# Kernel tuning notes

Measured on AMD Instinct MI355X. Metric: run time of the kernel, lower is better.

## Reference

```python
import jax, jax.numpy as jnp
import numpy as np

B, C, L = 32, 8, 2048
K, S = 512, 64  # num_shapelets, shapelets_size


def setup_inputs() -> dict:
    key = jax.random.key(0)
    k1, k2 = jax.random.split(key)
    x = jax.random.normal(k1, (B, C, L), dtype=jnp.float32)
    shapelets = jax.random.normal(k2, (C, K, S), dtype=jnp.float32)
    return {"x": x, "shapelets": shapelets}


def reference(x, shapelets):
    # x: [B, C, L]; shapelets: [C, K, S]
    s = shapelets.shape[-1]
    n_dims = x.shape[1]
    W = x.shape[2] - s + 1  # number of sliding windows
    # unfold(2, S, 1): gather overlapping windows -> [B, C, W, S]
    idx = jnp.arange(W)[:, None] + jnp.arange(s)[None, :]
    xw = x[:, :, idx]
    # L2-normalize windows along window length (clamp min like torch)
    xw = xw / jnp.maximum(jnp.linalg.norm(xw, axis=-1, keepdims=True), 1e-8)
    # L2-normalize shapelets along length
    sn = shapelets / jnp.maximum(jnp.linalg.norm(shapelets, axis=-1, keepdims=True), 1e-8)
    # matmul [B,C,W,S] @ [C,S,K] then sum over C, fused into one einsum -> [B, W, K]
    sim = jnp.einsum('bcws,cks->bwk', xw, sn) / n_dims
    sim = jax.nn.relu(sim)
    # max over window positions -> [B, K]; keep the singleton channel dim like torch ([B,1,K])
    out = jnp.max(sim, axis=1)
    return out[:, None, :]
```

## Files before the change

### kernel.cpp

```cpp
#include <hip/hip_runtime.h>


#define B_ 32
#define C_ 8
#define L_ 2048
#define K_ 512
#define S_ 64
#define W_ 1985
#define TW 64

typedef _Float16 f16x8 __attribute__((ext_vector_type(8)));
typedef float f32x4 __attribute__((ext_vector_type(4)));
typedef float f32x4u __attribute__((ext_vector_type(4), aligned(4)));

__global__ __launch_bounds__(256)
void prep_k(const float* __restrict__ x, const float* __restrict__ sh,
            _Float16* __restrict__ Bp, float* __restrict__ invn,
            float* __restrict__ out) {
    __shared__ float xr[L_];
    const int tid = threadIdx.x;
    const int blk = blockIdx.x;

    if (blk < 128) {
        const int sb   = blk * 4 + (tid >> 6);
        const int c    = sb >> 6;
        const int ks   = (sb >> 5) & 1;
        const int nt   = sb & 31;
        const int lane = tid & 63;
        const int ncol = lane & 15, quad = lane >> 4;
        const int q    = nt * 16 + ncol;

        const float4* sp = (const float4*)(sh + (size_t)(c * K_ + q) * S_);
        float ss = 0.f;
        #pragma unroll
        for (int i = 0; i < 4; ++i) {
            float4 v = sp[quad * 4 + i];
            ss += v.x * v.x + v.y * v.y + v.z * v.z + v.w * v.w;
        }
        ss += __shfl_xor(ss, 16);
        ss += __shfl_xor(ss, 32);
        float inv = 1.f / fmaxf(sqrtf(ss), 1e-8f);

        float4 u0 = sp[ks * 8 + quad * 2];
        float4 u1 = sp[ks * 8 + quad * 2 + 1];
        f16x8 o;
        o[0] = (_Float16)(u0.x * inv); o[1] = (_Float16)(u0.y * inv);
        o[2] = (_Float16)(u0.z * inv); o[3] = (_Float16)(u0.w * inv);
        o[4] = (_Float16)(u1.x * inv); o[5] = (_Float16)(u1.y * inv);
        o[6] = (_Float16)(u1.z * inv); o[7] = (_Float16)(u1.w * inv);
        ((f16x8*)Bp)[((c * 2 + ks) * 32 + nt) * 64 + lane] = o;
    } else {
        const int r = blk - 128;
        const float* xp = x + (size_t)r * L_;
        for (int i = tid; i < L_ / 4; i += 256)
            ((float4*)xr)[i] = ((const float4*)xp)[i];
        __syncthreads();

        float* ivp = invn + (size_t)r * L_;
        const int w0 = tid * 8;
        float ss = 0.f;
        if (w0 < W_) {
            #pragma unroll
            for (int j = 0; j < S_; ++j) { float v = xr[w0 + j]; ss += v * v; }
        }
        #pragma unroll
        for (int u = 0; u < 8; ++u) {
            int w = w0 + u;
            float o = 0.f;
            if (u > 0 && w < W_)
                ss += xr[w + 63] * xr[w + 63] - xr[w - 1] * xr[w - 1];
            if (w < W_) o = 0.125f / fmaxf(sqrtf(ss), 1e-8f);
            if (w < L_) ivp[w] = o;
        }
        if (r < 64) out[r * 256 + tid] = 0.f;
    }
}

__global__ __launch_bounds__(256, 3)
void mcs_k(const float* __restrict__ x, const _Float16* __restrict__ Bp,
           const float* __restrict__ invn, float* __restrict__ out) {
    __shared__ float invs[C_ * TW];
    __shared__ f16x8 Ah[2][8 * 64];

    const int wt  = blockIdx.x;
    const int ng  = blockIdx.y;
    const int b   = blockIdx.z;
    const int w0  = wt * TW;
    const int tid = threadIdx.x;
    const int lane = tid & 63;
    const int wv   = tid >> 6;
    const int quad = lane >> 4;

    for (int i = tid; i < C_ * TW; i += 256) {
        int c = i >> 6, w = i & 63;
        invs[i] = invn[(size_t)(b * C_ + c) * L_ + w0 + w];
    }

    auto build = [&](int cN, int bufN) {
        const float* xrow = x + (size_t)(b * C_ + cN) * L_;
        #pragma unroll
        for (int it = 0; it < 2; ++it) {
            int i   = tid + it * 256;
            int f   = i >> 6, l = i & 63;
            int mt  = f >> 1, ks = f & 1;
            int row = l & 15, qd = l >> 4;
            int m   = mt * 16 + row;
            int p   = w0 + m + ks * 32 + qd * 8;
            int pc  = p <= L_ - 8 ? p : L_ - 8;
            f32x4u v0 = *(const f32x4u*)(xrow + pc);
            f32x4u v1 = *(const f32x4u*)(xrow + pc + 4);
            float iv = invs[cN * TW + m];
            f16x8 o;
            o[0] = (_Float16)(v0[0] * iv); o[1] = (_Float16)(v0[1] * iv);
            o[2] = (_Float16)(v0[2] * iv); o[3] = (_Float16)(v0[3] * iv);
            o[4] = (_Float16)(v1[0] * iv); o[5] = (_Float16)(v1[1] * iv);
            o[6] = (_Float16)(v1[2] * iv); o[7] = (_Float16)(v1[3] * iv);
            Ah[bufN][f * 64 + l] = o;
        }
    };

    __syncthreads();
    build(0, 0);
    __syncthreads();

    f32x4 acc[4][4];
    #pragma unroll
    for (int mt = 0; mt < 4; ++mt)
        #pragma unroll
        for (int nt = 0; nt < 4; ++nt)
            acc[mt][nt] = (f32x4){0.f, 0.f, 0.f, 0.f};

    #pragma unroll 2
    for (int c = 0; c < C_; ++c) {
        const int buf = c & 1;
        if (c + 1 < C_) build(c + 1, buf ^ 1);

        #pragma unroll
        for (int ks = 0; ks < 2; ++ks) {
            f16x8 af[4], bf[4];
            const f16x8* bpp = (const f16x8*)Bp +
                ((c * 2 + ks) * 32 + ng * 16 + wv * 4) * 64 + lane;
            #pragma unroll
            for (int nt = 0; nt < 4; ++nt) bf[nt] = bpp[nt * 64];
            #pragma unroll
            for (int mt = 0; mt < 4; ++mt) af[mt] = Ah[buf][(mt * 2 + ks) * 64 + lane];
            #pragma unroll
            for (int nt = 0; nt < 4; ++nt)
                #pragma unroll
                for (int mt = 0; mt < 4; ++mt)
                    acc[mt][nt] = __builtin_amdgcn_mfma_f32_16x16x32_f16(
                        af[mt], bf[nt], acc[mt][nt], 0, 0, 0);
        }
        __syncthreads();
    }

    #pragma unroll
    for (int nt = 0; nt < 4; ++nt) {
        float m = 0.f;
        #pragma unroll
        for (int mt = 0; mt < 4; ++mt)
            #pragma unroll
            for (int r = 0; r < 4; ++r)
                m = fmaxf(m, acc[mt][nt][r]);
        m = fmaxf(m, __shfl_xor(m, 16));
        m = fmaxf(m, __shfl_xor(m, 32));
        if (lane < 16)
            atomicMax((unsigned int*)(out + b * K_ + ng * 256 + wv * 64 + nt * 16 + lane),
                      __float_as_uint(m));
    }
}

extern "C" void kernel_launch(void* const* d_in, const int* in_sizes, int n_in,
                              void* d_out, int out_size, void* d_ws, size_t ws_size,
                              hipStream_t stream) {
    const float* x  = (const float*)d_in[0];
    const float* sh = (const float*)d_in[1];
    float* out = (float*)d_out;
    _Float16* Bp  = (_Float16*)d_ws;
    float* invn   = (float*)((char*)d_ws + (size_t)K_ * 512 * sizeof(_Float16));

    prep_k<<<dim3(384), dim3(256), 0, stream>>>(x, sh, Bp, invn, out);
    mcs_k<<<dim3(32, 2, B_), dim3(256), 0, stream>>>(x, Bp, invn, out);
}
```

Baseline: 106.1 us.

## Switch to 32x32x16 MFMA tiles and process channel pairs per stage

Replaces the 16x16x32 f16 MFMA tiling with 32x32x16 MFMA, re-laying out the prepacked shapelet fragments and the LDS window fragments to match the new operand format. Each pipeline stage now builds two channels at once into a larger double-buffered LDS tile, halving the number of barriers in the channel loop. The aim is fewer operand loads per FLOP and better MFMA throughput, at the cost of more LDS per block and possibly reduced occupancy.

```diff
diff --git a/kernel.cpp b/kernel.cpp
--- a/kernel.cpp
+++ b/kernel.cpp
@@ -10,7 +10,7 @@
 #define TW 64
 
 typedef _Float16 f16x8 __attribute__((ext_vector_type(8)));
-typedef float f32x4 __attribute__((ext_vector_type(4)));
+typedef float f32x16 __attribute__((ext_vector_type(16)));
 typedef float f32x4u __attribute__((ext_vector_type(4), aligned(4)));
 
 __global__ __launch_bounds__(256)
@@ -24,31 +24,31 @@
     if (blk < 128) {
         const int sb   = blk * 4 + (tid >> 6);
         const int c    = sb >> 6;
-        const int ks   = (sb >> 5) & 1;
-        const int nt   = sb & 31;
+        const int kq   = (sb >> 4) & 3;
+        const int nt   = sb & 15;
         const int lane = tid & 63;
-        const int ncol = lane & 15, quad = lane >> 4;
-        const int q    = nt * 16 + ncol;
+        const int n    = lane & 31;
+        const int half = lane >> 5;
+        const int q    = nt * 32 + n;
 
         const float4* sp = (const float4*)(sh + (size_t)(c * K_ + q) * S_);
         float ss = 0.f;
         #pragma unroll
-        for (int i = 0; i < 4; ++i) {
-            float4 v = sp[quad * 4 + i];
+        for (int i = 0; i < 8; ++i) {
+            float4 v = sp[half * 8 + i];
             ss += v.x * v.x + v.y * v.y + v.z * v.z + v.w * v.w;
         }
-        ss += __shfl_xor(ss, 16);
         ss += __shfl_xor(ss, 32);
         float inv = 1.f / fmaxf(sqrtf(ss), 1e-8f);
 
-        float4 u0 = sp[ks * 8 + quad * 2];
-        float4 u1 = sp[ks * 8 + quad * 2 + 1];
+        float4 u0 = sp[kq * 4 + half * 2];
+        float4 u1 = sp[kq * 4 + half * 2 + 1];
         f16x8 o;
         o[0] = (_Float16)(u0.x * inv); o[1] = (_Float16)(u0.y * inv);
         o[2] = (_Float16)(u0.z * inv); o[3] = (_Float16)(u0.w * inv);
         o[4] = (_Float16)(u1.x * inv); o[5] = (_Float16)(u1.y * inv);
         o[6] = (_Float16)(u1.z * inv); o[7] = (_Float16)(u1.w * inv);
-        ((f16x8*)Bp)[((c * 2 + ks) * 32 + nt) * 64 + lane] = o;
+        ((f16x8*)Bp)[((c * 4 + kq) * 16 + nt) * 64 + lane] = o;
     } else {
         const int r = blk - 128;
         const float* xp = x + (size_t)r * L_;
@@ -80,7 +80,7 @@
 void mcs_k(const float* __restrict__ x, const _Float16* __restrict__ Bp,
            const float* __restrict__ invn, float* __restrict__ out) {
     __shared__ float invs[C_ * TW];
-    __shared__ f16x8 Ah[2][8 * 64];
+    __shared__ f16x8 Ah[2][16 * 64];
 
     const int wt  = blockIdx.x;
     const int ng  = blockIdx.y;
@@ -89,33 +89,32 @@
     const int tid = threadIdx.x;
     const int lane = tid & 63;
     const int wv   = tid >> 6;
-    const int quad = lane >> 4;
 
     for (int i = tid; i < C_ * TW; i += 256) {
         int c = i >> 6, w = i & 63;
         invs[i] = invn[(size_t)(b * C_ + c) * L_ + w0 + w];
     }
 
-    auto build = [&](int cN, int bufN) {
-        const float* xrow = x + (size_t)(b * C_ + cN) * L_;
+    auto build = [&](int cp, int buf) {
+        const int c0 = cp * 2;
         #pragma unroll
-        for (int it = 0; it < 2; ++it) {
-            int i   = tid + it * 256;
-            int f   = i >> 6, l = i & 63;
-            int mt  = f >> 1, ks = f & 1;
-            int row = l & 15, qd = l >> 4;
-            int m   = mt * 16 + row;
-            int p   = w0 + m + ks * 32 + qd * 8;
-            int pc  = p <= L_ - 8 ? p : L_ - 8;
+        for (int it = 0; it < 4; ++it) {
+            int i  = tid + it * 256;
+            int f  = i >> 6, l = i & 63;
+            int ch = f >> 3, mt = (f >> 2) & 1, ks = f & 3;
+            int m  = mt * 32 + (l & 31);
+            int p  = w0 + m + ks * 16 + (l >> 5) * 8;
+            int pc = p <= L_ - 8 ? p : L_ - 8;
+            const float* xrow = x + (size_t)(b * C_ + c0 + ch) * L_;
             f32x4u v0 = *(const f32x4u*)(xrow + pc);
             f32x4u v1 = *(const f32x4u*)(xrow + pc + 4);
-            float iv = invs[cN * TW + m];
+            float iv = invs[(c0 + ch) * TW + m];
             f16x8 o;
             o[0] = (_Float16)(v0[0] * iv); o[1] = (_Float16)(v0[1] * iv);
             o[2] = (_Float16)(v0[2] * iv); o[3] = (_Float16)(v0[3] * iv);
             o[4] = (_Float16)(v1[0] * iv); o[5] = (_Float16)(v1[1] * iv);
             o[6] = (_Float16)(v1[2] * iv); o[7] = (_Float16)(v1[3] * iv);
-            Ah[bufN][f * 64 + l] = o;
+            Ah[buf][f * 64 + l] = o;
         }
     };
 
@@ -123,49 +122,54 @@
     build(0, 0);
     __syncthreads();
 
-    f32x4 acc[4][4];
+    f32x16 acc[2][2];
     #pragma unroll
-    for (int mt = 0; mt < 4; ++mt)
+    for (int mt = 0; mt < 2; ++mt)
         #pragma unroll
-        for (int nt = 0; nt < 4; ++nt)
-            acc[mt][nt] = (f32x4){0.f, 0.f, 0.f, 0.f};
+        for (int nt = 0; nt < 2; ++nt)
+            #pragma unroll
+            for (int r = 0; r < 16; ++r) acc[mt][nt][r] = 0.f;
 
-    #pragma unroll 2
-    for (int c = 0; c < C_; ++c) {
-        const int buf = c & 1;
-        if (c + 1 < C_) build(c + 1, buf ^ 1);
+    #pragma unroll 1
+    for (int cp = 0; cp < 4; ++cp) {
+        const int buf = cp & 1;
+        if (cp + 1 < 4) build(cp + 1, buf ^ 1);
 
         #pragma unroll
-        for (int ks = 0; ks < 2; ++ks) {
-            f16x8 af[4], bf[4];
-            const f16x8* bpp = (const f16x8*)Bp +
-                ((c * 2 + ks) * 32 + ng * 16 + wv * 4) * 64 + lane;
+        for (int ch = 0; ch < 2; ++ch) {
+            const int c = cp * 2 + ch;
             #pragma unroll
-            for (int nt = 0; nt < 4; ++nt) bf[nt] = bpp[nt * 64];
-            #pragma unroll
-            for (int mt = 0; mt < 4; ++mt) af[mt] = Ah[buf][(mt * 2 + ks) * 64 + lane];
-            #pragma unroll
-            for (int nt = 0; nt < 4; ++nt)
+            for (int ks = 0; ks < 4; ++ks) {
+                f16x8 af[2], bf[2];
                 #pragma unroll
-                for (int mt = 0; mt < 4; ++mt)
-                    acc[mt][nt] = __builtin_amdgcn_mfma_f32_16x16x32_f16(
-                        af[mt], bf[nt], acc[mt][nt], 0, 0, 0);
+                for (int mt = 0; mt < 2; ++mt)
+                    af[mt] = Ah[buf][(ch * 8 + mt * 4 + ks) * 64 + lane];
+                const f16x8* bpp = (const f16x8*)Bp +
+                    ((c * 4 + ks) * 16 + ng * 8 + wv * 2) * 64 + lane;
+                #pragma unroll
+                for (int nt = 0; nt < 2; ++nt) bf[nt] = bpp[nt * 64];
+                #pragma unroll
+                for (int nt = 0; nt < 2; ++nt)
+                    #pragma unroll
+                    for (int mt = 0; mt < 2; ++mt)
+                        acc[mt][nt] = __builtin_amdgcn_mfma_f32_32x32x16_f16(
+                            af[mt], bf[nt], acc[mt][nt], 0, 0, 0);
+            }
         }
         __syncthreads();
     }
 
     #pragma unroll
-    for (int nt = 0; nt < 4; ++nt) {
+    for (int nt = 0; nt < 2; ++nt) {
         float m = 0.f;
         #pragma unroll
-        for (int mt = 0; mt < 4; ++mt)
+        for (int mt = 0; mt < 2; ++mt)
             #pragma unroll
-            for (int r = 0; r < 4; ++r)
+            for (int r = 0; r < 16; ++r)
                 m = fmaxf(m, acc[mt][nt][r]);
-        m = fmaxf(m, __shfl_xor(m, 16));
         m = fmaxf(m, __shfl_xor(m, 32));
-        if (lane < 16)
-            atomicMax((unsigned int*)(out + b * K_ + ng * 256 + wv * 64 + nt * 16 + lane),
+        if (lane < 32)
+            atomicMax((unsigned int*)(out + b * K_ + ng * 256 + wv * 64 + nt * 32 + lane),
                       __float_as_uint(m));
     }
 }
```

After: 100.7 us. 1.05x faster.
